# Optimization experiments

Measured on AMD Instinct MI355X. Metric: run time of the kernel, lower is better.

Reference implementation:

```python
import jax, jax.numpy as jnp
import numpy as np

D = 128; DFF = 256; NH = 4; HD = D // NH
B = 8; T = 1024
PAIRS = [(0, 1), (1, 2), (0, 2)]  # (ABSTRACT,DYNAMIC),(DYNAMIC,CONCRETE),(ABSTRACT,CONCRETE)
BW = 0.5 / 3.0   # bridge_weight / len(BRIDGE_PAIRS)
LB_W = 0.01


def _hex_np():
    # itertools.product([-1,1], repeat=6): index i = 6-bit binary of i, MSB first, 0->-1
    bits = (np.arange(64)[:, None] >> np.arange(5, -1, -1)) & 1
    return (bits * 2.0 - 1.0).astype(np.float32)


def _anchors_np():
    h = _hex_np()
    idx = {'GEO': 0, 'HYDRO': 18, 'PYRO': 45, 'AERO': 6, 'COSMO': 27, 'NOOS': 63}
    a = (h[idx['NOOS']] + h[idx['COSMO']]) / 2.0   # ABSTRACT
    d = (h[idx['AERO']] + h[idx['PYRO']]) / 2.0    # DYNAMIC
    c = (h[idx['GEO']] + h[idx['HYDRO']]) / 2.0    # CONCRETE
    return np.stack([a, d, c]).astype(np.float32)


def _ln(x, g, b, eps=1e-5):
    m = x.mean(-1, keepdims=True)
    v = ((x - m) ** 2).mean(-1, keepdims=True)
    return (x - m) * jax.lax.rsqrt(v + eps) * g + b


def _mha(q, kv, in_w, out_w):
    # torch nn.MultiheadAttention, bias=False, batch_first
    Bq, Tq, _ = q.shape
    wq, wk, wv = in_w[:D], in_w[D:2 * D], in_w[2 * D:]
    Q = (q @ wq.T).reshape(Bq, Tq, NH, HD)
    K = (kv @ wk.T).reshape(Bq, Tq, NH, HD)
    V = (kv @ wv.T).reshape(Bq, Tq, NH, HD)
    scores = jnp.einsum('bqhd,bkhd->bhqk', Q, K) / jnp.sqrt(jnp.float32(HD))
    attn = jax.nn.softmax(scores, axis=-1)
    o = jnp.einsum('bhqk,bkhd->bqhd', attn, V).reshape(Bq, Tq, D)
    return o @ out_w.T


def setup_inputs() -> dict:
    key = jax.random.key(0)
    ks = iter(jax.random.split(key, 40))
    r = lambda shape, s=0.02: jax.random.normal(next(ks), shape, dtype=jnp.float32) * s
    return {
        'x': jax.random.normal(next(ks), (B, T, D), dtype=jnp.float32),
        'gr_norm_g': jnp.ones((D,), jnp.float32), 'gr_norm_b': jnp.zeros((D,), jnp.float32),
        'q6_w': r((6, D), 0.1),
        'log_temp': jnp.log(jnp.float32(0.5)),
        'grp_norm_g': jnp.ones((3, D), jnp.float32), 'grp_norm_b': jnp.zeros((3, D), jnp.float32),
        'grp_proj_w': r((3, 2, D), 0.1), 'grp_proj_b': jnp.zeros((3, 2), jnp.float32),
        'me_norm_g': jnp.ones((6, D), jnp.float32), 'me_norm_b': jnp.zeros((6, D), jnp.float32),
        'me_gate_w': r((6, DFF, D)), 'me_val_w': r((6, DFF, D)), 'me_out_w': r((6, D, DFF)),
        'br_in_w': r((3, 3 * D, D)), 'br_out_w': r((3, D, D)),
        'br_nq_g': jnp.ones((3, D), jnp.float32), 'br_nq_b': jnp.zeros((3, D), jnp.float32),
        'br_nkv_g': jnp.ones((3, D), jnp.float32), 'br_nkv_b': jnp.zeros((3, D), jnp.float32),
        'br_nffn_g': jnp.ones((3, D), jnp.float32), 'br_nffn_b': jnp.zeros((3, D), jnp.float32),
        'br_gate_w': r((3, 2 * D, D)), 'br_val_w': r((3, 2 * D, D)), 'br_ffn_out_w': r((3, D, 2 * D)),
        'br_gate': jnp.full((3,), -2.0, dtype=jnp.float32),
        'out_norm_g': jnp.ones((D,), jnp.float32), 'out_norm_b': jnp.zeros((D,), jnp.float32),
        'out_w': r((D, D)),
    }


def reference(x, gr_norm_g, gr_norm_b, q6_w, log_temp, grp_norm_g, grp_norm_b,
              grp_proj_w, grp_proj_b, me_norm_g, me_norm_b, me_gate_w, me_val_w,
              me_out_w, br_in_w, br_out_w, br_nq_g, br_nq_b, br_nkv_g, br_nkv_b,
              br_nffn_g, br_nffn_b, br_gate_w, br_val_w, br_ffn_out_w, br_gate,
              out_norm_g, out_norm_b, out_w):
    hexg = jnp.asarray(_hex_np())        # (64, 6)
    anchors = jnp.asarray(_anchors_np())  # (3, 6)

    # ---- GlobalRouter ----
    h = _ln(x, gr_norm_g, gr_norm_b)
    soft_bits = jnp.tanh(h @ q6_w.T)                       # (B,T,6)
    sim = soft_bits @ hexg.T                               # (B,T,64)
    temp = jnp.clip(jnp.exp(log_temp), 0.1, 5.0)
    hex_w = jax.nn.softmax(sim / temp, axis=-1)
    soft_hex = hex_w @ hexg                                # (B,T,6)
    group_weights = jax.nn.softmax(soft_hex @ anchors.T, axis=-1)  # (B,T,3)
    mw = group_weights.mean(axis=(0, 1))
    lb_total = -(mw * jnp.log(mw + 1e-8)).sum()

    # ---- all 6 micro experts (per-expert LayerNorm shares x's stats) ----
    m = x.mean(-1, keepdims=True)
    v = ((x - m) ** 2).mean(-1, keepdims=True)
    xn = (x - m) * jax.lax.rsqrt(v + 1e-5)                 # (B,T,D)
    hme = xn[None] * me_norm_g[:, None, None, :] + me_norm_b[:, None, None, :]  # (6,B,T,D)
    gate = jax.nn.silu(jnp.einsum('ebtd,efd->ebtf', hme, me_gate_w))
    val = jnp.einsum('ebtd,efd->ebtf', hme, me_val_w)
    eo = jnp.einsum('ebtf,edf->ebtd', gate * val, me_out_w)  # (6,B,T,D)

    # ---- per-group routing (2 experts each, top_k=2) ----
    group_outs = []
    for g in range(3):  # groups ordered [ABSTRACT, DYNAMIC, CONCRETE]; experts [2g, 2g+1]
        hg = xn * grp_norm_g[g] + grp_norm_b[g]
        logits = hg @ grp_proj_w[g].T + grp_proj_b[g]      # (B,T,2)
        w = jax.nn.softmax(logits, axis=-1)
        vals, idx = jax.lax.top_k(w, 2)                    # k = min(top_k=2, n=2)
        sparse = (jax.nn.one_hot(idx, 2, dtype=w.dtype) * vals[..., None]).sum(-2)
        sparse = sparse / (sparse.sum(-1, keepdims=True) + 1e-8)
        mwg = w.mean(axis=(0, 1))
        lb_total = lb_total - (mwg * jnp.log(mwg + 1e-8)).sum()
        go = sparse[..., 0:1] * eo[2 * g] + sparse[..., 1:2] * eo[2 * g + 1]
        group_outs.append(group_weights[..., g:g + 1] * go)

    # ---- bridge experts ----
    bridge_sum = jnp.zeros_like(x)
    for i, (a, b) in enumerate(PAIRS):
        xq, xk = group_outs[a], group_outs[b]
        qn = _ln(xq, br_nq_g[i], br_nq_b[i])
        kvn = _ln(xk, br_nkv_g[i], br_nkv_b[i])
        xb = xq + _mha(qn, kvn, br_in_w[i], br_out_w[i])
        hb = _ln(xb, br_nffn_g[i], br_nffn_b[i])
        ff = (jax.nn.silu(hb @ br_gate_w[i].T) * (hb @ br_val_w[i].T)) @ br_ffn_out_w[i].T
        xb = (xb + ff) * jax.nn.sigmoid(br_gate[i])
        bridge_sum = bridge_sum + BW * xb

    combined = group_outs[0] + group_outs[1] + group_outs[2] + bridge_sum
    out = _ln(combined, out_norm_g, out_norm_b) @ out_w.T
    return out, lb_total * LB_W
```

## Files before the change

kernel.cpp:

```cpp
#include <hip/hip_runtime.h>
#include <math.h>

#define DD    128
#define DFF   256
#define NHH   4
#define HDD   32
#define BB    8
#define TT    1024
#define NTOK  (BB*TT)
#define LDK   72
#define QKVN  384

#define WB_MEGATE 0
#define WB_MEVAL  196608
#define WB_MEOUT  393216
#define WB_BRIN   589824
#define WB_BROUT  737280
#define WB_BRG    786432
#define WB_BRV    884736
#define WB_BRF    983040
#define WB_OUTW   1081344
#define WB_TOT    1097728

typedef __bf16 bf16x8 __attribute__((ext_vector_type(8)));
typedef float  f32x4  __attribute__((ext_vector_type(4)));

__device__ __forceinline__ float wsum(float v){
#pragma unroll
  for(int o=32;o>0;o>>=1) v += __shfl_xor(v,o,64);
  return v;
}
__device__ __forceinline__ float wmaxr(float v){
#pragma unroll
  for(int o=32;o>0;o>>=1) v = fmaxf(v,__shfl_xor(v,o,64));
  return v;
}
__device__ __forceinline__ unsigned short f2bf(float x){
  __bf16 h = (__bf16)x;
  unsigned short u;
  __builtin_memcpy(&u, &h, 2);
  return u;
}

__device__ __forceinline__ void stage16(const float* __restrict__ gp,
                                        unsigned short* __restrict__ dst){
  float4 f0 = *reinterpret_cast<const float4*>(gp);
  float4 f1 = *reinterpret_cast<const float4*>(gp+4);
  float4 f2 = *reinterpret_cast<const float4*>(gp+8);
  float4 f3 = *reinterpret_cast<const float4*>(gp+12);
  float f[16] = {f0.x,f0.y,f0.z,f0.w, f1.x,f1.y,f1.z,f1.w,
                 f2.x,f2.y,f2.z,f2.w, f3.x,f3.y,f3.z,f3.w};
  unsigned short h[16];
#pragma unroll
  for(int j=0;j<16;j++) h[j] = f2bf(f[j]);
  *reinterpret_cast<uint4*>(dst)   = *reinterpret_cast<const uint4*>(h);
  *reinterpret_cast<uint4*>(dst+8) = *reinterpret_cast<const uint4*>(h+8);
}

__device__ __forceinline__ void stage16bf(const unsigned short* __restrict__ gp,
                                          unsigned short* __restrict__ dst){
  const uint4* s = reinterpret_cast<const uint4*>(gp);
  *reinterpret_cast<uint4*>(dst)   = s[0];
  *reinterpret_cast<uint4*>(dst+8) = s[1];
}

__device__ __forceinline__ void stageLN(const float* __restrict__ fr,
                                        float mean, float rstd,
                                        const float* __restrict__ g,
                                        const float* __restrict__ b,
                                        unsigned short* __restrict__ dst){
  unsigned short h[16];
#pragma unroll
  for(int j=0;j<16;j++){
    float y = (fr[j]-mean)*rstd*g[j] + b[j];
    h[j] = f2bf(y);
  }
  *reinterpret_cast<uint4*>(dst)   = *reinterpret_cast<const uint4*>(h);
  *reinterpret_cast<uint4*>(dst+8) = *reinterpret_cast<const uint4*>(h+8);
}

__global__ __launch_bounds__(256) void wconv(
    const float* __restrict__ a0, const float* __restrict__ a1, const float* __restrict__ a2,
    const float* __restrict__ a3, const float* __restrict__ a4, const float* __restrict__ a5,
    const float* __restrict__ a6, const float* __restrict__ a7, const float* __restrict__ a8,
    unsigned short* __restrict__ dst, float qsc){
  size_t i = ((size_t)blockIdx.x*256 + threadIdx.x)*4;
  if(i >= WB_TOT) return;
  const float* s; size_t off = i; float sc = 1.0f;
  if(i < WB_MEVAL){ s=a0; }
  else if(i < WB_MEOUT){ s=a1; off = i-WB_MEVAL; }
  else if(i < WB_BRIN ){ s=a2; off = i-WB_MEOUT; }
  else if(i < WB_BROUT){ s=a3; off = i-WB_BRIN;
    int row = (int)(off>>7); if((row % 384) < 128) sc = qsc; }
  else if(i < WB_BRG ){ s=a4; off = i-WB_BROUT; }
  else if(i < WB_BRV ){ s=a5; off = i-WB_BRG; }
  else if(i < WB_BRF ){ s=a6; off = i-WB_BRV; }
  else if(i < WB_OUTW){ s=a7; off = i-WB_BRF; }
  else { s=a8; off = i-WB_OUTW; }
  float4 v = *reinterpret_cast<const float4*>(s + off);
  unsigned short h4[4] = {f2bf(v.x*sc), f2bf(v.y*sc), f2bf(v.z*sc), f2bf(v.w*sc)};
  *reinterpret_cast<uint2*>(dst + i) = *reinterpret_cast<const uint2*>(h4);
}

__global__ __launch_bounds__(256) void routing_kernel(
    const float* __restrict__ x,
    const float* __restrict__ gr_g, const float* __restrict__ gr_b,
    const float* __restrict__ q6,   const float* __restrict__ logtemp,
    const float* __restrict__ grp_g,const float* __restrict__ grp_b,
    const float* __restrict__ gpw,  const float* __restrict__ gpb,
    float* __restrict__ gw_out, float* __restrict__ coef, float* __restrict__ part){
  __shared__ float sp[4][9];
  int lane = threadIdx.x & 63;
  int wv   = threadIdx.x >> 6;
  int t    = (blockIdx.x<<2) + wv;
  const float* xr = x + (size_t)t*DD;
  float r0 = xr[lane], r1 = xr[lane+64];
  float mn = wsum(r0+r1) * (1.0f/DD);
  float d0 = r0-mn, d1 = r1-mn;
  float vv = wsum(d0*d0 + d1*d1) * (1.0f/DD);
  float rstd = rsqrtf(vv + 1e-5f);
  float x0 = d0*rstd, x1 = d1*rstd;
  float h0 = x0*gr_g[lane]+gr_b[lane];
  float h1 = x1*gr_g[lane+64]+gr_b[lane+64];
  float sb[6];
#pragma unroll
  for(int j=0;j<6;j++){
    float p = h0*q6[j*DD+lane] + h1*q6[j*DD+lane+64];
    sb[j] = tanhf(wsum(p));
  }
  float sim = 0.f;
#pragma unroll
  for(int j=0;j<6;j++) sim += ((lane>>(5-j))&1) ? sb[j] : -sb[j];
  float temp = expf(logtemp[0]); temp = fminf(fmaxf(temp,0.1f),5.0f);
  float mx = wmaxr(sim);
  float p  = expf((sim-mx)/temp);
  float w  = p / wsum(p);
  float sh[6];
#pragma unroll
  for(int j=0;j<6;j++) sh[j] = wsum(((lane>>(5-j))&1) ? w : -w);
  const float A0[6]={0,1,1,0,1,1}, A1[6]={0,-1,0,1,0,0}, A2[6]={-1,0,-1,-1,0,-1};
  float l0=0,l1=0,l2=0;
#pragma unroll
  for(int j=0;j<6;j++){ l0+=sh[j]*A0[j]; l1+=sh[j]*A1[j]; l2+=sh[j]*A2[j]; }
  float m3 = fmaxf(l0,fmaxf(l1,l2));
  float e0=expf(l0-m3), e1=expf(l1-m3), e2=expf(l2-m3);
  float inv3 = 1.0f/(e0+e1+e2);
  float g0=e0*inv3, g1=e1*inv3, g2=e2*inv3;
  if(lane==0){ gw_out[t*3]=g0; gw_out[t*3+1]=g1; gw_out[t*3+2]=g2; }
  float gwv[3]={g0,g1,g2};
  float pw[6];
#pragma unroll
  for(int g=0; g<3; g++){
    float hg0 = x0*grp_g[g*DD+lane]    + grp_b[g*DD+lane];
    float hg1 = x1*grp_g[g*DD+lane+64] + grp_b[g*DD+lane+64];
    float q0 = wsum(hg0*gpw[(g*2+0)*DD+lane] + hg1*gpw[(g*2+0)*DD+lane+64]) + gpb[g*2+0];
    float q1 = wsum(hg0*gpw[(g*2+1)*DD+lane] + hg1*gpw[(g*2+1)*DD+lane+64]) + gpb[g*2+1];
    float mm = fmaxf(q0,q1);
    float a0 = expf(q0-mm), a1 = expf(q1-mm);
    float inv = 1.0f/(a0+a1);
    float w0 = a0*inv, w1 = a1*inv;
    pw[g*2]=w0; pw[g*2+1]=w1;
    float invs = 1.0f/(w0+w1+1e-8f);
    if(lane==0){
      coef[(size_t)(2*g  )*NTOK + t] = gwv[g]*w0*invs;
      coef[(size_t)(2*g+1)*NTOK + t] = gwv[g]*w1*invs;
    }
  }
  if(lane==0){
    sp[wv][0]=g0; sp[wv][1]=g1; sp[wv][2]=g2;
#pragma unroll
    for(int k=0;k<6;k++) sp[wv][3+k]=pw[k];
  }
  __syncthreads();
  if(threadIdx.x<9){
    part[blockIdx.x*9+threadIdx.x] =
      sp[0][threadIdx.x]+sp[1][threadIdx.x]+sp[2][threadIdx.x]+sp[3][threadIdx.x];
  }
}

__global__ __launch_bounds__(256) void lb_kernel(const float* __restrict__ part, float* __restrict__ outlb){
  __shared__ float sm[4][9];
  float acc[9] = {};
  for(int i=threadIdx.x; i<2048; i+=256){
#pragma unroll
    for(int c=0;c<9;c++) acc[c] += part[i*9+c];
  }
#pragma unroll
  for(int c=0;c<9;c++) acc[c] = wsum(acc[c]);
  int wv = threadIdx.x>>6, lane = threadIdx.x&63;
  if(lane==0){
#pragma unroll
    for(int c=0;c<9;c++) sm[wv][c]=acc[c];
  }
  __syncthreads();
  if(threadIdx.x==0){
    const float invN = 1.0f/(float)NTOK;
    float lb=0;
#pragma unroll
    for(int c=0;c<9;c++){
      float s = sm[0][c]+sm[1][c]+sm[2][c]+sm[3][c];
      float mw = s*invN;
      lb -= mw*logf(mw+1e-8f);
    }
    outlb[0] = lb*0.01f;
  }
}

template<int MODE,int LN,int ABF,int OBF,int PSEL,int RSEL,int SUM,int QKV>
__global__ __launch_bounds__(256) void gemm_mfma(
    const void* __restrict__ Ap, const unsigned short* __restrict__ W, void* __restrict__ Cp,
    int M, int N, int K,
    const float* __restrict__ sv, const float* __restrict__ bv,
    const float* __restrict__ resid, const float* __restrict__ gptr,
    size_t az, size_t wz, size_t cz, size_t pz, size_t rz, size_t gz){
  __shared__ unsigned short As[64*LDK];
  __shared__ unsigned short Ws[64*LDK];
  const int z = blockIdx.z;
  const float* A = (const float*)Ap;
  const unsigned short* Ab = (const unsigned short*)Ap;
  if(QKV){
    bool isQ = (blockIdx.x < 2);
    int s = isQ ? ((z==1)?1:0) : ((z==0)?1:2);
    A += (size_t)s*NTOK*DD;
    if(!isQ){ sv = resid; bv = gptr; }
  } else if(PSEL==0){ A += z*az; Ab += z*az; }
  else if(PSEL==1){ int s = (z==1)?1:0; A += (size_t)s*NTOK*DD; Ab += (size_t)s*NTOK*DD; }
  else            { int s = (z==0)?1:2; A += (size_t)s*NTOK*DD; Ab += (size_t)s*NTOK*DD; }
  W += z*wz;
  float* C = (float*)Cp + z*cz;
  unsigned short* Cb = (unsigned short*)Cp + z*cz;
  const float* rs = resid;
  if(RSEL==0) rs += z*rz;
  else { int s = (z==1)?1:0; rs += (size_t)s*NTOK*DD; }
  sv += z*pz; bv += z*pz;
  const float* gp2 = gptr + z*gz;
  int tid  = threadIdx.x;
  int m0   = blockIdx.y*64, n0 = blockIdx.x*64;
  int w    = tid>>6, lane = tid&63;
  int wr   = (w>>1)*32, wc = (w&1)*32;
  int r    = tid>>2, seg = (tid&3)*16;
  f32x4 acc[2][2] = {};
  auto step = [&](){
#pragma unroll
    for(int kk=0;kk<64;kk+=32){
      int ko = kk + (lane>>4)*8;
      bf16x8 a0 = *reinterpret_cast<const bf16x8*>(&As[(wr    + (lane&15))*LDK + ko]);
      bf16x8 a1 = *reinterpret_cast<const bf16x8*>(&As[(wr+16 + (lane&15))*LDK + ko]);
      bf16x8 b0 = *reinterpret_cast<const bf16x8*>(&Ws[(wc    + (lane&15))*LDK + ko]);
      bf16x8 b1 = *reinterpret_cast<const bf16x8*>(&Ws[(wc+16 + (lane&15))*LDK + ko]);
      acc[0][0] = __builtin_amdgcn_mfma_f32_16x16x32_bf16(a0,b0,acc[0][0],0,0,0);
      acc[0][1] = __builtin_amdgcn_mfma_f32_16x16x32_bf16(a0,b1,acc[0][1],0,0,0);
      acc[1][0] = __builtin_amdgcn_mfma_f32_16x16x32_bf16(a1,b0,acc[1][0],0,0,0);
      acc[1][1] = __builtin_amdgcn_mfma_f32_16x16x32_bf16(a1,b1,acc[1][1],0,0,0);
    }
  };
  if(LN){
    float fr[32]; float mean, rstd;
    if(SUM){
#pragma unroll
      for(int j=0;j<32;j++) fr[j]=0.f;
#pragma unroll
      for(int s=0;s<3;s++){
        const float* r1 = A     + (size_t)s*NTOK*DD + (size_t)(m0+r)*K + seg;
        const float* r2 = resid + (size_t)s*NTOK*DD + (size_t)(m0+r)*K + seg;
#pragma unroll
        for(int j=0;j<4;j++){
          float4 v1 = *reinterpret_cast<const float4*>(r1 + j*4);
          float4 v2 = *reinterpret_cast<const float4*>(r2 + j*4);
          fr[j*4]+=v1.x+v2.x; fr[j*4+1]+=v1.y+v2.y; fr[j*4+2]+=v1.z+v2.z; fr[j*4+3]+=v1.w+v2.w;
          float4 w1 = *reinterpret_cast<const float4*>(r1 + 64 + j*4);
          float4 w2 = *reinterpret_cast<const float4*>(r2 + 64 + j*4);
          fr[16+j*4]+=w1.x+w2.x; fr[16+j*4+1]+=w1.y+w2.y; fr[16+j*4+2]+=w1.z+w2.z; fr[16+j*4+3]+=w1.w+w2.w;
        }
      }
    } else {
      const float* arow = A + (size_t)(m0+r)*K + seg;
#pragma unroll
      for(int j=0;j<4;j++) *reinterpret_cast<float4*>(&fr[j*4])    = *reinterpret_cast<const float4*>(arow + j*4);
#pragma unroll
      for(int j=0;j<4;j++) *reinterpret_cast<float4*>(&fr[16+j*4]) = *reinterpret_cast<const float4*>(arow + 64 + j*4);
    }
    float s1=0.f, s2=0.f;
#pragma unroll
    for(int j=0;j<32;j++){ s1 += fr[j]; s2 += fr[j]*fr[j]; }
    s1 += __shfl_xor(s1,1,64); s1 += __shfl_xor(s1,2,64);
    s2 += __shfl_xor(s2,1,64); s2 += __shfl_xor(s2,2,64);
    mean = s1*(1.0f/DD);
    float var = s2*(1.0f/DD) - mean*mean;
    rstd = rsqrtf(var + 1e-5f);
#pragma unroll
    for(int kh=0; kh<2; ++kh){
      __syncthreads();
      stageLN(fr + kh*16, mean, rstd, sv + kh*64 + seg, bv + kh*64 + seg, &As[r*LDK + seg]);
      stage16bf(W + (size_t)(n0+r)*K + kh*64 + seg, &Ws[r*LDK + seg]);
      __syncthreads();
      step();
    }
  } else {
    for(int k0=0;k0<K;k0+=64){
      __syncthreads();
      if(ABF) stage16bf(Ab + (size_t)(m0+r)*K + k0 + seg, &As[r*LDK + seg]);
      else    stage16(A  + (size_t)(m0+r)*K + k0 + seg, &As[r*LDK + seg]);
      stage16bf(W + (size_t)(n0+r)*K + k0 + seg, &Ws[r*LDK + seg]);
      __syncthreads();
      step();
    }
  }
#pragma unroll
  for(int i=0;i<2;i++){
#pragma unroll
    for(int j=0;j<2;j++){
      int mb = m0 + wr + i*16 + (lane>>4)*4;
      int n  = n0 + wc + j*16 + (lane&15);
#pragma unroll
      for(int rg=0;rg<4;rg++){
        int m = mb + rg;
        float v = acc[i][j][rg];
        size_t o = (size_t)m*N + n;
        if(MODE==0){ if(OBF) Cb[o] = f2bf(v); else C[o] = v; }
        else if(MODE==3){ C[o] = rs[o] + v; }
        else if(MODE==5){
          float gs = (0.5f/3.0f)/(1.0f+expf(-gp2[0]));
          C[o] = gs*(rs[o]+v);
        }
      }
    }
  }
}

__global__ __launch_bounds__(256) void gemm_dual(
    const float* __restrict__ A, const unsigned short* __restrict__ G,
    const unsigned short* __restrict__ V,
    unsigned short* __restrict__ C, int M, int N, int K,
    const float* __restrict__ sv, const float* __restrict__ bv,
    size_t az, size_t wz, size_t cz, size_t pz){
  __shared__ unsigned short As[64*LDK];
  __shared__ unsigned short Gs[64*LDK];
  __shared__ unsigned short Vs[64*LDK];
  const int z = blockIdx.z;
  A += z*az; G += z*wz; V += z*wz; C += z*cz; sv += z*pz; bv += z*pz;
  int tid  = threadIdx.x;
  int m0   = blockIdx.y*64, n0 = blockIdx.x*64;
  int w    = tid>>6, lane = tid&63;
  int wr   = (w>>1)*32, wc = (w&1)*32;
  int r    = tid>>2, seg = (tid&3)*16;
  f32x4 accg[2][2] = {};
  f32x4 accv[2][2] = {};
  float fr[32]; float mean, rstd;
  {
    const float* arow = A + (size_t)(m0+r)*K + seg;
#pragma unroll
    for(int j=0;j<4;j++) *reinterpret_cast<float4*>(&fr[j*4])    = *reinterpret_cast<const float4*>(arow + j*4);
#pragma unroll
    for(int j=0;j<4;j++) *reinterpret_cast<float4*>(&fr[16+j*4]) = *reinterpret_cast<const float4*>(arow + 64 + j*4);
    float s1=0.f, s2=0.f;
#pragma unroll
    for(int j=0;j<32;j++){ s1 += fr[j]; s2 += fr[j]*fr[j]; }
    s1 += __shfl_xor(s1,1,64); s1 += __shfl_xor(s1,2,64);
    s2 += __shfl_xor(s2,1,64); s2 += __shfl_xor(s2,2,64);
    mean = s1*(1.0f/DD);
    float var = s2*(1.0f/DD) - mean*mean;
    rstd = rsqrtf(var + 1e-5f);
  }
#pragma unroll
  for(int kh=0; kh<2; ++kh){
    int k0 = kh*64;
    __syncthreads();
    stageLN(fr + kh*16, mean, rstd, sv + k0 + seg, bv + k0 + seg, &As[r*LDK + seg]);
    stage16bf(G + (size_t)(n0+r)*K + k0 + seg, &Gs[r*LDK + seg]);
    stage16bf(V + (size_t)(n0+r)*K + k0 + seg, &Vs[r*LDK + seg]);
    __syncthreads();
#pragma unroll
    for(int kk=0;kk<64;kk+=32){
      int ko = kk + (lane>>4)*8;
      bf16x8 a0 = *reinterpret_cast<const bf16x8*>(&As[(wr    + (lane&15))*LDK + ko]);
      bf16x8 a1 = *reinterpret_cast<const bf16x8*>(&As[(wr+16 + (lane&15))*LDK + ko]);
      bf16x8 g0 = *reinterpret_cast<const bf16x8*>(&Gs[(wc    + (lane&15))*LDK + ko]);
      bf16x8 g1 = *reinterpret_cast<const bf16x8*>(&Gs[(wc+16 + (lane&15))*LDK + ko]);
      bf16x8 v0 = *reinterpret_cast<const bf16x8*>(&Vs[(wc    + (lane&15))*LDK + ko]);
      bf16x8 v1 = *reinterpret_cast<const bf16x8*>(&Vs[(wc+16 + (lane&15))*LDK + ko]);
      accg[0][0] = __builtin_amdgcn_mfma_f32_16x16x32_bf16(a0,g0,accg[0][0],0,0,0);
      accg[0][1] = __builtin_amdgcn_mfma_f32_16x16x32_bf16(a0,g1,accg[0][1],0,0,0);
      accg[1][0] = __builtin_amdgcn_mfma_f32_16x16x32_bf16(a1,g0,accg[1][0],0,0,0);
      accg[1][1] = __builtin_amdgcn_mfma_f32_16x16x32_bf16(a1,g1,accg[1][1],0,0,0);
      accv[0][0] = __builtin_amdgcn_mfma_f32_16x16x32_bf16(a0,v0,accv[0][0],0,0,0);
      accv[0][1] = __builtin_amdgcn_mfma_f32_16x16x32_bf16(a0,v1,accv[0][1],0,0,0);
      accv[1][0] = __builtin_amdgcn_mfma_f32_16x16x32_bf16(a1,v0,accv[1][0],0,0,0);
      accv[1][1] = __builtin_amdgcn_mfma_f32_16x16x32_bf16(a1,v1,accv[1][1],0,0,0);
    }
  }
#pragma unroll
  for(int i=0;i<2;i++){
#pragma unroll
    for(int j=0;j<2;j++){
      int mb = m0 + wr + i*16 + (lane>>4)*4;
      int n  = n0 + wc + j*16 + (lane&15);
#pragma unroll
      for(int rg=0;rg<4;rg++){
        float gg = accg[i][j][rg];
        float vv = accv[i][j][rg];
        float sg = gg/(1.0f+expf(-gg));
        C[(size_t)(mb+rg)*N + n] = f2bf(sg*vv);
      }
    }
  }
}

__global__ __launch_bounds__(256) void gemm_moe2(
    const unsigned short* __restrict__ Ab, const unsigned short* __restrict__ Wb,
    float* __restrict__ Cb, const float* __restrict__ coef){
  __shared__ unsigned short As0[64*LDK];
  __shared__ unsigned short As1[64*LDK];
  __shared__ unsigned short Ws0[64*LDK];
  __shared__ unsigned short Ws1[64*LDK];
  const int g = blockIdx.z;
  const unsigned short* A0 = Ab + (size_t)(2*g)*NTOK*DFF;
  const unsigned short* A1 = A0 + (size_t)NTOK*DFF;
  const unsigned short* W0 = Wb + (size_t)(2*g)*DD*DFF;
  const unsigned short* W1 = W0 + (size_t)DD*DFF;
  float* C = Cb + (size_t)g*NTOK*DD;
  const float* c0 = coef + (size_t)(2*g)*NTOK;
  const float* c1 = c0 + NTOK;
  int tid  = threadIdx.x;
  int m0   = blockIdx.y*64, n0 = blockIdx.x*64;
  int w    = tid>>6, lane = tid&63;
  int wr   = (w>>1)*32, wc = (w&1)*32;
  int r    = tid>>2, seg = (tid&3)*16;
  f32x4 a0acc[2][2] = {};
  f32x4 a1acc[2][2] = {};
  for(int k0=0;k0<DFF;k0+=64){
    __syncthreads();
    stage16bf(A0 + (size_t)(m0+r)*DFF + k0 + seg, &As0[r*LDK + seg]);
    stage16bf(A1 + (size_t)(m0+r)*DFF + k0 + seg, &As1[r*LDK + seg]);
    stage16bf(W0 + (size_t)(n0+r)*DFF + k0 + seg, &Ws0[r*LDK + seg]);
    stage16bf(W1 + (size_t)(n0+r)*DFF + k0 + seg, &Ws1[r*LDK + seg]);
    __syncthreads();
#pragma unroll
    for(int kk=0;kk<64;kk+=32){
      int ko = kk + (lane>>4)*8;
      bf16x8 x00 = *reinterpret_cast<const bf16x8*>(&As0[(wr    + (lane&15))*LDK + ko]);
      bf16x8 x01 = *reinterpret_cast<const bf16x8*>(&As0[(wr+16 + (lane&15))*LDK + ko]);
      bf16x8 x10 = *reinterpret_cast<const bf16x8*>(&As1[(wr    + (lane&15))*LDK + ko]);
      bf16x8 x11 = *reinterpret_cast<const bf16x8*>(&As1[(wr+16 + (lane&15))*LDK + ko]);
      bf16x8 w00 = *reinterpret_cast<const bf16x8*>(&Ws0[(wc    + (lane&15))*LDK + ko]);
      bf16x8 w01 = *reinterpret_cast<const bf16x8*>(&Ws0[(wc+16 + (lane&15))*LDK + ko]);
      bf16x8 w10 = *reinterpret_cast<const bf16x8*>(&Ws1[(wc    + (lane&15))*LDK + ko]);
      bf16x8 w11 = *reinterpret_cast<const bf16x8*>(&Ws1[(wc+16 + (lane&15))*LDK + ko]);
      a0acc[0][0] = __builtin_amdgcn_mfma_f32_16x16x32_bf16(x00,w00,a0acc[0][0],0,0,0);
      a0acc[0][1] = __builtin_amdgcn_mfma_f32_16x16x32_bf16(x00,w01,a0acc[0][1],0,0,0);
      a0acc[1][0] = __builtin_amdgcn_mfma_f32_16x16x32_bf16(x01,w00,a0acc[1][0],0,0,0);
      a0acc[1][1] = __builtin_amdgcn_mfma_f32_16x16x32_bf16(x01,w01,a0acc[1][1],0,0,0);
      a1acc[0][0] = __builtin_amdgcn_mfma_f32_16x16x32_bf16(x10,w10,a1acc[0][0],0,0,0);
      a1acc[0][1] = __builtin_amdgcn_mfma_f32_16x16x32_bf16(x10,w11,a1acc[0][1],0,0,0);
      a1acc[1][0] = __builtin_amdgcn_mfma_f32_16x16x32_bf16(x11,w10,a1acc[1][0],0,0,0);
      a1acc[1][1] = __builtin_amdgcn_mfma_f32_16x16x32_bf16(x11,w11,a1acc[1][1],0,0,0);
    }
  }
#pragma unroll
  for(int i=0;i<2;i++){
#pragma unroll
    for(int j=0;j<2;j++){
      int mb = m0 + wr + i*16 + (lane>>4)*4;
      int n  = n0 + wc + j*16 + (lane&15);
#pragma unroll
      for(int rg=0;rg<4;rg++){
        int m = mb + rg;
        C[(size_t)m*DD + n] = c0[m]*a0acc[i][j][rg] + c1[m]*a1acc[i][j][rg];
      }
    }
  }
}

#define PSW(row) (((row)&8)<<1)
#define VSW(row) ((((row)>>3)&3)<<3)
__global__ __launch_bounds__(512) void attn_fused(
    const unsigned short* __restrict__ qkv,
    unsigned short* __restrict__ obuf){
  __shared__ __align__(16) unsigned short Ks[2][64*40];
  __shared__ __align__(16) unsigned short Vt[2][32*72];
  __shared__ __align__(16) unsigned short Vones[16*72];
  __shared__ __align__(16) unsigned short Ps[8][16*72];
  const int tid = threadIdx.x;
  const int w = tid>>6, lane = tid&63;
  const int lr = lane&15, lg = lane>>4;
  const int n_  = blockIdx.x;
  const int kx  = n_ & 7, jx = n_ >> 3;
  const int grp = kx*12 + (jx>>3);
  const int bx  = jx & 7;
  const int h   = grp & 3;
  const int b   = (grp>>2) & 7;
  const int br  = grp >> 5;
  const int qtok0 = b*TT + bx*128 + w*16;
  for(int idx=tid; idx<16*72; idx+=512)
    Vones[idx] = (idx < 64) ? (unsigned short)0x3F80 : (unsigned short)0;
  const unsigned short* qp = qkv + (size_t)br*NTOK*QKVN + (size_t)(qtok0 + lr)*QKVN + h*HDD + lg*8;
  bf16x8 qa = *reinterpret_cast<const bf16x8*>(qp);
  f32x4 o0 = {}, o1 = {}, o2 = {};
  float m[4] = {-1e30f,-1e30f,-1e30f,-1e30f};
  const unsigned short* KVbase = qkv + (size_t)br*NTOK*QKVN + (size_t)(b*TT)*QKVN + DD + h*HDD;
  const int skey = tid>>3, sseg = (tid&7)*4;

  {
    const unsigned short* s0 = KVbase + (size_t)skey*QKVN + sseg;
    uint2 kv = *reinterpret_cast<const uint2*>(s0);
    uint2 vv = *reinterpret_cast<const uint2*>(s0 + DD);
    *reinterpret_cast<uint2*>(&Ks[0][skey*40+sseg]) = kv;
    unsigned short vs[4];
    *reinterpret_cast<uint2*>(vs) = vv;
    const int kc = skey ^ VSW(sseg);
    Vt[0][(sseg  )*72+kc]=vs[0]; Vt[0][(sseg+1)*72+kc]=vs[1];
    Vt[0][(sseg+2)*72+kc]=vs[2]; Vt[0][(sseg+3)*72+kc]=vs[3];
  }
  __syncthreads();

  for(int t=0; t<16; t++){
    const int cur = t & 1;
    uint2 kn, vn;
    if(t < 15){
      const unsigned short* s0 = KVbase + (size_t)((t+1)*64 + skey)*QKVN + sseg;
      kn = *reinterpret_cast<const uint2*>(s0);
      vn = *reinterpret_cast<const uint2*>(s0 + DD);
    }
    f32x4 s[4];
#pragma unroll
    for(int f=0;f<4;f++){
      bf16x8 kb = *reinterpret_cast<const bf16x8*>(&Ks[cur][(f*16+lr)*40 + lg*8]);
      f32x4 z = {};
      s[f] = __builtin_amdgcn_mfma_f32_16x16x32_bf16(qa,kb,z,0,0,0);
    }
    float tmax[4]; bool need=false;
#pragma unroll
    for(int r=0;r<4;r++){
      tmax[r] = fmaxf(fmaxf(s[0][r],s[1][r]),fmaxf(s[2][r],s[3][r]));
      need = need || (tmax[r] > m[r] + 8.0f);
    }
    if(__any(need)){
#pragma unroll
      for(int r=0;r<4;r++){
        float t2 = tmax[r];
#pragma unroll
        for(int off=1;off<16;off<<=1) t2 = fmaxf(t2,__shfl_xor(t2,off,64));
        float nm = fmaxf(m[r],t2);
        float sc = __builtin_amdgcn_exp2f(m[r]-nm);
        m[r] = nm; o0[r] *= sc; o1[r] *= sc; o2[r] *= sc;
      }
    }
#pragma unroll
    for(int r=0;r<4;r++){
      const int q = lg*4+r;
      const int cw = PSW(q);
#pragma unroll
      for(int f=0;f<4;f++){
        float p = __builtin_amdgcn_exp2f(s[f][r]-m[r]);
        Ps[w][q*72 + ((f*16+lr)^cw)] = f2bf(p);
      }
    }
    const int pw_ = PSW(lr);
    bf16x8 pa0 = *reinterpret_cast<const bf16x8*>(&Ps[w][lr*72 + ((lg*8   )^pw_)]);
    bf16x8 pa1 = *reinterpret_cast<const bf16x8*>(&Ps[w][lr*72 + ((lg*8+32)^pw_)]);
    {
      const int r_ = lr, vw = VSW(r_);
      bf16x8 vb0 = *reinterpret_cast<const bf16x8*>(&Vt[cur][r_*72 + ((lg*8   )^vw)]);
      bf16x8 vb1 = *reinterpret_cast<const bf16x8*>(&Vt[cur][r_*72 + ((lg*8+32)^vw)]);
      o0 = __builtin_amdgcn_mfma_f32_16x16x32_bf16(pa0,vb0,o0,0,0,0);
      o0 = __builtin_amdgcn_mfma_f32_16x16x32_bf16(pa1,vb1,o0,0,0,0);
    }
    {
      const int r_ = 16+lr, vw = VSW(r_);
      bf16x8 vb0 = *reinterpret_cast<const bf16x8*>(&Vt[cur][(r_-16)*72 + ((lg*8   )^vw)+16*72]);
      bf16x8 vb1 = *reinterpret_cast<const bf16x8*>(&Vt[cur][(r_-16)*72 + ((lg*8+32)^vw)+16*72]);
      o1 = __builtin_amdgcn_mfma_f32_16x16x32_bf16(pa0,vb0,o1,0,0,0);
      o1 = __builtin_amdgcn_mfma_f32_16x16x32_bf16(pa1,vb1,o1,0,0,0);
    }
    {
      const int r_ = 32+lr, vw = VSW(r_);
      bf16x8 vb0 = *reinterpret_cast<const bf16x8*>(&Vones[lr*72 + ((lg*8   )^vw)]);
      bf16x8 vb1 = *reinterpret_cast<const bf16x8*>(&Vones[lr*72 + ((lg*8+32)^vw)]);
      o2 = __builtin_amdgcn_mfma_f32_16x16x32_bf16(pa0,vb0,o2,0,0,0);
      o2 = __builtin_amdgcn_mfma_f32_16x16x32_bf16(pa1,vb1,o2,0,0,0);
    }
    if(t < 15){
      const int nb = cur ^ 1;
      *reinterpret_cast<uint2*>(&Ks[nb][skey*40+sseg]) = kn;
      unsigned short vs[4];
      *reinterpret_cast<uint2*>(vs) = vn;
      const int kc = skey ^ VSW(sseg);
      Vt[nb][(sseg  )*72+kc]=vs[0]; Vt[nb][(sseg+1)*72+kc]=vs[1];
      Vt[nb][(sseg+2)*72+kc]=vs[2]; Vt[nb][(sseg+3)*72+kc]=vs[3];
    }
    __syncthreads();
  }
#pragma unroll
  for(int r=0;r<4;r++){
    float lsr = __shfl(o2[r], lane & 48, 64);
    float inv = 1.0f/lsr;
    int row = qtok0 + lg*4 + r;
    unsigned short* orow = obuf + (size_t)br*NTOK*DD + (size_t)row*DD + h*HDD;
    orow[lr]    = f2bf(o0[r]*inv);
    orow[16+lr] = f2bf(o1[r]*inv);
  }
}

extern "C" void kernel_launch(void* const* d_in, const int* in_sizes, int n_in,
                              void* d_out, int out_size, void* d_ws, size_t ws_size,
                              hipStream_t stream){
  (void)in_sizes; (void)n_in; (void)out_size; (void)ws_size;
  const float* x       = (const float*)d_in[0];
  const float* gr_g    = (const float*)d_in[1];
  const float* gr_b    = (const float*)d_in[2];
  const float* q6_w    = (const float*)d_in[3];
  const float* logtemp = (const float*)d_in[4];
  const float* grp_g   = (const float*)d_in[5];
  const float* grp_b   = (const float*)d_in[6];
  const float* gpw     = (const float*)d_in[7];
  const float* gpb     = (const float*)d_in[8];
  const float* me_g    = (const float*)d_in[9];
  const float* me_b    = (const float*)d_in[10];
  const float* me_gate = (const float*)d_in[11];
  const float* me_val  = (const float*)d_in[12];
  const float* me_out  = (const float*)d_in[13];
  const float* br_in   = (const float*)d_in[14];
  const float* br_outw = (const float*)d_in[15];
  const float* nq_g    = (const float*)d_in[16];
  const float* nq_b    = (const float*)d_in[17];
  const float* nkv_g   = (const float*)d_in[18];
  const float* nkv_b   = (const float*)d_in[19];
  const float* nff_g   = (const float*)d_in[20];
  const float* nff_b   = (const float*)d_in[21];
  const float* brg_w   = (const float*)d_in[22];
  const float* brv_w   = (const float*)d_in[23];
  const float* brf_w   = (const float*)d_in[24];
  const float* br_gate = (const float*)d_in[25];
  const float* on_g    = (const float*)d_in[26];
  const float* on_b    = (const float*)d_in[27];
  const float* out_w   = (const float*)d_in[28];
  float* out = (float*)d_out;
  float* ws  = (float*)d_ws;

  float* coef  = ws;
  float* part  = ws + 65536;
  unsigned short* gvb6 = (unsigned short*)(ws + 131072);
  float* go    = ws + 6731072;
  unsigned short* qkv  = (unsigned short*)(ws + 9900000);
  unsigned short* obuf = (unsigned short*)(ws + 14700000);
  unsigned short* wbf  = (unsigned short*)(ws + 21400000);
  float* xb    = ws + 23000000;
  unsigned short* gvb2 = (unsigned short*)(ws + 26200000);
  float* bsum  = ws + 29400000;
  float* gw    = ws + 32700000;

  const float qscale = 0.17677669529663687f * 1.4426950408889634f;

  wconv<<<1072,256,0,stream>>>(me_gate, me_val, me_out, br_in, br_outw,
                               brg_w, brv_w, brf_w, out_w, wbf, qscale);

  routing_kernel<<<2048,256,0,stream>>>(x, gr_g, gr_b, q6_w, logtemp,
                                        grp_g, grp_b, gpw, gpb, gw, coef, part);
  lb_kernel<<<1,256,0,stream>>>(part, out + 1048576);

  gemm_dual<<<dim3(4,128,6),256,0,stream>>>(x, wbf+WB_MEGATE, wbf+WB_MEVAL, gvb6,
      NTOK,DFF,DD, me_g, me_b, 0, (size_t)DFF*DD, (size_t)NTOK*DFF, DD);
  gemm_moe2<<<dim3(2,128,3),256,0,stream>>>(gvb6, wbf+WB_MEOUT, go, coef);

  gemm_mfma<0,1,0,1,0,0,0,1><<<dim3(6,128,3),256,0,stream>>>(go, wbf+WB_BRIN, qkv,
      NTOK,QKVN,DD, nq_g, nq_b, nkv_g, nkv_b,
      0, (size_t)QKVN*DD, (size_t)NTOK*QKVN, DD, 0, 0);
  attn_fused<<<768,512,0,stream>>>(qkv, obuf);
  gemm_mfma<3,0,1,0,0,1,0,0><<<dim3(2,128,3),256,0,stream>>>(obuf, wbf+WB_BROUT, xb,
      NTOK,DD,DD, nullptr, nullptr, go, nullptr,
      (size_t)NTOK*DD, (size_t)DD*DD, (size_t)NTOK*DD, 0, 0, 0);
  gemm_dual<<<dim3(4,128,3),256,0,stream>>>(xb, wbf+WB_BRG, wbf+WB_BRV, gvb2,
      NTOK,2*DD,DD, nff_g, nff_b, (size_t)NTOK*DD, (size_t)2*DD*DD, (size_t)NTOK*2*DD, DD);
  gemm_mfma<5,0,1,0,0,0,0,0><<<dim3(2,128,3),256,0,stream>>>(gvb2, wbf+WB_BRF, bsum,
      NTOK,DD,2*DD, nullptr, nullptr, xb, br_gate,
      (size_t)NTOK*2*DD, (size_t)DD*2*DD, (size_t)NTOK*DD, 0, (size_t)NTOK*DD, 1);

  gemm_mfma<0,1,0,0,0,0,1,0><<<dim3(2,128,1),256,0,stream>>>(go, wbf+WB_OUTW, out,
      NTOK,DD,DD, on_g, on_b, bsum, nullptr,
      0, 0, 0, 0, 0, 0);
}
```

Baseline: 184.1 us.

## Store intermediate activations in bf16 and accumulate bridge output into group outputs

```diff
diff --git a/kernel.cpp b/kernel.cpp
--- a/kernel.cpp
+++ b/kernel.cpp
@@ -40,6 +40,10 @@
   unsigned short u;
   __builtin_memcpy(&u, &h, 2);
   return u;
+}
+__device__ __forceinline__ float bf2f(unsigned short u){
+  unsigned int x = ((unsigned int)u)<<16;
+  float f; __builtin_memcpy(&f, &x, 4); return f;
 }
 
 __device__ __forceinline__ void stage16(const float* __restrict__ gp,
@@ -206,12 +210,12 @@
   }
 }
 
-template<int MODE,int LN,int ABF,int OBF,int PSEL,int RSEL,int SUM,int QKV>
+template<int MODE,int LN,int ABF,int OBF,int PSEL,int RSEL,int SUM,int QKV,int RBF>
 __global__ __launch_bounds__(256) void gemm_mfma(
     const void* __restrict__ Ap, const unsigned short* __restrict__ W, void* __restrict__ Cp,
     int M, int N, int K,
     const float* __restrict__ sv, const float* __restrict__ bv,
-    const float* __restrict__ resid, const float* __restrict__ gptr,
+    const void* __restrict__ resid, const float* __restrict__ gptr,
     size_t az, size_t wz, size_t cz, size_t pz, size_t rz, size_t gz){
   __shared__ unsigned short As[64*LDK];
   __shared__ unsigned short Ws[64*LDK];
@@ -221,17 +225,18 @@
   if(QKV){
     bool isQ = (blockIdx.x < 2);
     int s = isQ ? ((z==1)?1:0) : ((z==0)?1:2);
-    A += (size_t)s*NTOK*DD;
-    if(!isQ){ sv = resid; bv = gptr; }
+    A  += (size_t)s*NTOK*DD;
+    Ab += (size_t)s*NTOK*DD;
+    if(!isQ){ sv = (const float*)resid; bv = gptr; }
   } else if(PSEL==0){ A += z*az; Ab += z*az; }
-  else if(PSEL==1){ int s = (z==1)?1:0; A += (size_t)s*NTOK*DD; Ab += (size_t)s*NTOK*DD; }
-  else            { int s = (z==0)?1:2; A += (size_t)s*NTOK*DD; Ab += (size_t)s*NTOK*DD; }
+  else { int s = (z==1)?1:0; A += (size_t)s*NTOK*DD; Ab += (size_t)s*NTOK*DD; }
   W += z*wz;
   float* C = (float*)Cp + z*cz;
   unsigned short* Cb = (unsigned short*)Cp + z*cz;
-  const float* rs = resid;
-  if(RSEL==0) rs += z*rz;
-  else { int s = (z==1)?1:0; rs += (size_t)s*NTOK*DD; }
+  const float* rsf = (const float*)resid;
+  const unsigned short* rsb = (const unsigned short*)resid;
+  if(RSEL==0){ rsf += z*rz; rsb += z*rz; }
+  else { int s = (z==1)?1:0; rsf += (size_t)s*NTOK*DD; rsb += (size_t)s*NTOK*DD; }
   sv += z*pz; bv += z*pz;
   const float* gp2 = gptr + z*gz;
   int tid  = threadIdx.x;
@@ -261,18 +266,14 @@
       for(int j=0;j<32;j++) fr[j]=0.f;
 #pragma unroll
       for(int s=0;s<3;s++){
-        const float* r1 = A     + (size_t)s*NTOK*DD + (size_t)(m0+r)*K + seg;
-        const float* r2 = resid + (size_t)s*NTOK*DD + (size_t)(m0+r)*K + seg;
-#pragma unroll
-        for(int j=0;j<4;j++){
-          float4 v1 = *reinterpret_cast<const float4*>(r1 + j*4);
-          float4 v2 = *reinterpret_cast<const float4*>(r2 + j*4);
-          fr[j*4]+=v1.x+v2.x; fr[j*4+1]+=v1.y+v2.y; fr[j*4+2]+=v1.z+v2.z; fr[j*4+3]+=v1.w+v2.w;
-          float4 w1 = *reinterpret_cast<const float4*>(r1 + 64 + j*4);
-          float4 w2 = *reinterpret_cast<const float4*>(r2 + 64 + j*4);
-          fr[16+j*4]+=w1.x+w2.x; fr[16+j*4+1]+=w1.y+w2.y; fr[16+j*4+2]+=w1.z+w2.z; fr[16+j*4+3]+=w1.w+w2.w;
-        }
+        const unsigned short* r1 = Ab + (size_t)s*NTOK*DD + (size_t)(m0+r)*K + seg;
+#pragma unroll
+        for(int j=0;j<16;j++){ fr[j] += bf2f(r1[j]); fr[16+j] += bf2f(r1[64+j]); }
       }
+    } else if(ABF){
+      const unsigned short* arow = Ab + (size_t)(m0+r)*K + seg;
+#pragma unroll
+      for(int j=0;j<16;j++){ fr[j] = bf2f(arow[j]); fr[16+j] = bf2f(arow[64+j]); }
     } else {
       const float* arow = A + (size_t)(m0+r)*K + seg;
 #pragma unroll
@@ -318,18 +319,25 @@
         float v = acc[i][j][rg];
         size_t o = (size_t)m*N + n;
         if(MODE==0){ if(OBF) Cb[o] = f2bf(v); else C[o] = v; }
-        else if(MODE==3){ C[o] = rs[o] + v; }
+        else if(MODE==3){
+          float rv = RBF ? bf2f(rsb[o]) : rsf[o];
+          float res = rv + v;
+          if(OBF) Cb[o] = f2bf(res); else C[o] = res;
+        }
         else if(MODE==5){
           float gs = (0.5f/3.0f)/(1.0f+expf(-gp2[0]));
-          C[o] = gs*(rs[o]+v);
+          float rv = RBF ? bf2f(rsb[o]) : rsf[o];
+          if(OBF) Cb[o] = f2bf(bf2f(Cb[o]) + gs*(rv+v));
+          else    C[o] += gs*(rv+v);
         }
       }
     }
   }
 }
 
+template<int ABF>
 __global__ __launch_bounds__(256) void gemm_dual(
-    const float* __restrict__ A, const unsigned short* __restrict__ G,
+    const void* __restrict__ Ap, const unsigned short* __restrict__ G,
     const unsigned short* __restrict__ V,
     unsigned short* __restrict__ C, int M, int N, int K,
     const float* __restrict__ sv, const float* __restrict__ bv,
@@ -338,7 +346,9 @@
   __shared__ unsigned short Gs[64*LDK];
   __shared__ unsigned short Vs[64*LDK];
   const int z = blockIdx.z;
-  A += z*az; G += z*wz; V += z*wz; C += z*cz; sv += z*pz; bv += z*pz;
+  const float* A = (const float*)Ap + z*az;
+  const unsigned short* Ab = (const unsigned short*)Ap + z*az;
+  G += z*wz; V += z*wz; C += z*cz; sv += z*pz; bv += z*pz;
   int tid  = threadIdx.x;
   int m0   = blockIdx.y*64, n0 = blockIdx.x*64;
   int w    = tid>>6, lane = tid&63;
@@ -347,12 +357,18 @@
   f32x4 accg[2][2] = {};
   f32x4 accv[2][2] = {};
   float fr[32]; float mean, rstd;
+  if(ABF){
+    const unsigned short* arow = Ab + (size_t)(m0+r)*K + seg;
+#pragma unroll
+    for(int j=0;j<16;j++){ fr[j] = bf2f(arow[j]); fr[16+j] = bf2f(arow[64+j]); }
+  } else {
+    const float* arow = A + (size_t)(m0+r)*K + seg;
+#pragma unroll
+    for(int j=0;j<4;j++) *reinterpret_cast<float4*>(&fr[j*4])    = *reinterpret_cast<const float4*>(arow + j*4);
+#pragma unroll
+    for(int j=0;j<4;j++) *reinterpret_cast<float4*>(&fr[16+j*4]) = *reinterpret_cast<const float4*>(arow + 64 + j*4);
+  }
   {
-    const float* arow = A + (size_t)(m0+r)*K + seg;
-#pragma unroll
-    for(int j=0;j<4;j++) *reinterpret_cast<float4*>(&fr[j*4])    = *reinterpret_cast<const float4*>(arow + j*4);
-#pragma unroll
-    for(int j=0;j<4;j++) *reinterpret_cast<float4*>(&fr[16+j*4]) = *reinterpret_cast<const float4*>(arow + 64 + j*4);
     float s1=0.f, s2=0.f;
 #pragma unroll
     for(int j=0;j<32;j++){ s1 += fr[j]; s2 += fr[j]*fr[j]; }
@@ -408,7 +424,7 @@
 
 __global__ __launch_bounds__(256) void gemm_moe2(
     const unsigned short* __restrict__ Ab, const unsigned short* __restrict__ Wb,
-    float* __restrict__ Cb, const float* __restrict__ coef){
+    unsigned short* __restrict__ Cb, const float* __restrict__ coef){
   __shared__ unsigned short As0[64*LDK];
   __shared__ unsigned short As1[64*LDK];
   __shared__ unsigned short Ws0[64*LDK];
@@ -418,7 +434,7 @@
   const unsigned short* A1 = A0 + (size_t)NTOK*DFF;
   const unsigned short* W0 = Wb + (size_t)(2*g)*DD*DFF;
   const unsigned short* W1 = W0 + (size_t)DD*DFF;
-  float* C = Cb + (size_t)g*NTOK*DD;
+  unsigned short* C = Cb + (size_t)g*NTOK*DD;
   const float* c0 = coef + (size_t)(2*g)*NTOK;
   const float* c1 = c0 + NTOK;
   int tid  = threadIdx.x;
@@ -465,7 +481,7 @@
 #pragma unroll
       for(int rg=0;rg<4;rg++){
         int m = mb + rg;
-        C[(size_t)m*DD + n] = c0[m]*a0acc[i][j][rg] + c1[m]*a1acc[i][j][rg];
+        C[(size_t)m*DD + n] = f2bf(c0[m]*a0acc[i][j][rg] + c1[m]*a1acc[i][j][rg]);
       }
     }
   }
@@ -640,13 +656,12 @@
   float* coef  = ws;
   float* part  = ws + 65536;
   unsigned short* gvb6 = (unsigned short*)(ws + 131072);
-  float* go    = ws + 6731072;
+  unsigned short* gob  = (unsigned short*)(ws + 6731072);
   unsigned short* qkv  = (unsigned short*)(ws + 9900000);
   unsigned short* obuf = (unsigned short*)(ws + 14700000);
   unsigned short* wbf  = (unsigned short*)(ws + 21400000);
-  float* xb    = ws + 23000000;
+  unsigned short* xbb  = (unsigned short*)(ws + 23000000);
   unsigned short* gvb2 = (unsigned short*)(ws + 26200000);
-  float* bsum  = ws + 29400000;
   float* gw    = ws + 32700000;
 
   const float qscale = 0.17677669529663687f * 1.4426950408889634f;
@@ -658,24 +673,24 @@
                                         grp_g, grp_b, gpw, gpb, gw, coef, part);
   lb_kernel<<<1,256,0,stream>>>(part, out + 1048576);
 
-  gemm_dual<<<dim3(4,128,6),256,0,stream>>>(x, wbf+WB_MEGATE, wbf+WB_MEVAL, gvb6,
+  gemm_dual<0><<<dim3(4,128,6),256,0,stream>>>(x, wbf+WB_MEGATE, wbf+WB_MEVAL, gvb6,
       NTOK,DFF,DD, me_g, me_b, 0, (size_t)DFF*DD, (size_t)NTOK*DFF, DD);
-  gemm_moe2<<<dim3(2,128,3),256,0,stream>>>(gvb6, wbf+WB_MEOUT, go, coef);
-
-  gemm_mfma<0,1,0,1,0,0,0,1><<<dim3(6,128,3),256,0,stream>>>(go, wbf+WB_BRIN, qkv,
+  gemm_moe2<<<dim3(2,128,3),256,0,stream>>>(gvb6, wbf+WB_MEOUT, gob, coef);
+
+  gemm_mfma<0,1,1,1,0,0,0,1,0><<<dim3(6,128,3),256,0,stream>>>(gob, wbf+WB_BRIN, qkv,
       NTOK,QKVN,DD, nq_g, nq_b, nkv_g, nkv_b,
       0, (size_t)QKVN*DD, (size_t)NTOK*QKVN, DD, 0, 0);
   attn_fused<<<768,512,0,stream>>>(qkv, obuf);
-  gemm_mfma<3,0,1,0,0,1,0,0><<<dim3(2,128,3),256,0,stream>>>(obuf, wbf+WB_BROUT, xb,
-      NTOK,DD,DD, nullptr, nullptr, go, nullptr,
+  gemm_mfma<3,0,1,1,0,1,0,0,1><<<dim3(2,128,3),256,0,stream>>>(obuf, wbf+WB_BROUT, xbb,
+      NTOK,DD,DD, nullptr, nullptr, gob, nullptr,
       (size_t)NTOK*DD, (size_t)DD*DD, (size_t)NTOK*DD, 0, 0, 0);
-  gemm_dual<<<dim3(4,128,3),256,0,stream>>>(xb, wbf+WB_BRG, wbf+WB_BRV, gvb2,
+  gemm_dual<1><<<dim3(4,128,3),256,0,stream>>>(xbb, wbf+WB_BRG, wbf+WB_BRV, gvb2,
       NTOK,2*DD,DD, nff_g, nff_b, (size_t)NTOK*DD, (size_t)2*DD*DD, (size_t)NTOK*2*DD, DD);
-  gemm_mfma<5,0,1,0,0,0,0,0><<<dim3(2,128,3),256,0,stream>>>(gvb2, wbf+WB_BRF, bsum,
-      NTOK,DD,2*DD, nullptr, nullptr, xb, br_gate,
+  gemm_mfma<5,0,1,1,0,0,0,0,1><<<dim3(2,128,3),256,0,stream>>>(gvb2, wbf+WB_BRF, gob,
+      NTOK,DD,2*DD, nullptr, nullptr, xbb, br_gate,
       (size_t)NTOK*2*DD, (size_t)DD*2*DD, (size_t)NTOK*DD, 0, (size_t)NTOK*DD, 1);
 
-  gemm_mfma<0,1,0,0,0,0,1,0><<<dim3(2,128,1),256,0,stream>>>(go, wbf+WB_OUTW, out,
-      NTOK,DD,DD, on_g, on_b, bsum, nullptr,
+  gemm_mfma<0,1,1,0,0,0,1,0,0><<<dim3(2,128,1),256,0,stream>>>(gob, wbf+WB_OUTW, out,
+      NTOK,DD,DD, on_g, on_b, nullptr, nullptr,
       0, 0, 0, 0, 0, 0);
 }
```

Result: faster. 168.8 us (-8.4%).
